# Performance work log

Measured on AMD Instinct MI355X. Metric: run time of the kernel, lower is better.

## Reference

```python
import jax, jax.numpy as jnp
import numpy as np

NDIR = 6      # build_tree.num_directions()
IDIM = 256
ODIM = 512
B, L, NCH = 8, 4096, 8192


def setup_inputs() -> dict:
    key = jax.random.key(0)
    ks = jax.random.split(key, 9)
    last = jax.random.normal(ks[0], (B, NCH, IDIM), dtype=jnp.float32)
    child_l = jax.random.randint(ks[1], (L,), 0, NCH, dtype=jnp.int32)
    child_r = jax.random.randint(ks[2], (L,), 0, NCH, dtype=jnp.int32)
    vec = jax.random.randint(ks[3], (B, L), 0, NCH, dtype=jnp.int32)
    drev = jax.random.randint(ks[4], (NCH,), 0, 2, dtype=jnp.int32)
    dmap = jax.random.randint(ks[5], (NCH,), 0, NDIR, dtype=jnp.int32)
    # merge FC params: ndir independent Linear(2*idim -> odim) + PReLU(init=relu_weight)
    scale = 1.0 / np.sqrt(2 * IDIM)
    W_merge = jax.random.uniform(ks[6], (NDIR, ODIM, 2 * IDIM), jnp.float32, -scale, scale)
    b_merge = jax.random.uniform(ks[7], (NDIR, ODIM), jnp.float32, -scale, scale)
    alpha_merge = jnp.full((NDIR,), 0.005, dtype=jnp.float32)  # PReLU weight (relu_weight)
    return {"last": last, "W_merge": W_merge, "b_merge": b_merge,
            "alpha_merge": alpha_merge, "child_l": child_l, "child_r": child_r,
            "vec": vec, "drev": drev, "dmap": dmap}


def reference(last, W_merge, b_merge, alpha_merge, child_l, child_r, vec, drev, dmap):
    # child gathers: [B, L, idim]
    lch = last[:, child_l]
    rch = last[:, child_r]
    # per-element direction-reverse blending
    d = drev[vec][:, :, None].astype(last.dtype)          # [B, L, 1]
    a = lch * (1.0 - d) + rch * d
    b = rch * (1.0 - d) + lch * d
    ans = jnp.concatenate([a, b], axis=-1)                # [B, L, 2*idim]
    # routed merge: compute all ndir linears, then select per element (ndir is small)
    y_all = jnp.einsum('bli,doi->bldo', ans, W_merge) + b_merge   # [B, L, ndir, odim]
    dir_idx = dmap[vec]                                   # [B, L] in [0, ndir)
    y = jnp.take_along_axis(y_all, dir_idx[:, :, None, None], axis=2)[:, :, 0]  # [B, L, odim]
    alpha = alpha_merge[dir_idx][:, :, None]              # per-element PReLU slope
    return jnp.where(y > 0, y, alpha * y)
```

## Files before the change

### kernel.cpp

```cpp
#include <hip/hip_runtime.h>
#include <hip/hip_bf16.h>

#define BB 8
#define LL 4096
#define NCH 8192
#define IDIM 256
#define KDIM 512
#define ODIM 512
#define NDIR 6
#define TOT (BB * LL)

#define CAP 8192
#define IDX_OFF 64
#define ROWS_OFF (64 + 8 * CAP)
#define WS_LAST_OFF (64 + 16 * CAP)
#define LAST_ELEMS (BB * NCH * IDIM)
#define W_ELEMS (NDIR * ODIM * KDIM)
#define N_LAST8 (LAST_ELEMS / 8)
#define N_W8 (W_ELEMS / 8)

#define GEMM_CHUNK 131

typedef short short8 __attribute__((ext_vector_type(8)));
typedef float floatx4 __attribute__((ext_vector_type(4)));

__device__ inline void async_copy16(const void* g, void* l) {
  __builtin_amdgcn_global_load_lds(
      (const __attribute__((address_space(1))) void*)g,
      (__attribute__((address_space(3))) void*)l, 16, 0, 0);
}

__device__ inline void cvt8(const float* __restrict__ src,
                            __hip_bfloat16* __restrict__ dst, int i) {
  const floatx4* s = (const floatx4*)src;
  floatx4 a = s[2 * i];
  floatx4 b = s[2 * i + 1];
  union { short8 v; __hip_bfloat16 h[8]; } u;
  u.h[0] = __float2bfloat16(a[0]); u.h[1] = __float2bfloat16(a[1]);
  u.h[2] = __float2bfloat16(a[2]); u.h[3] = __float2bfloat16(a[3]);
  u.h[4] = __float2bfloat16(b[0]); u.h[5] = __float2bfloat16(b[1]);
  u.h[6] = __float2bfloat16(b[2]); u.h[7] = __float2bfloat16(b[3]);
  ((short8*)dst)[i] = u.v;
}

__global__ __launch_bounds__(256) void prep_kernel(
    const float* __restrict__ last, const float* __restrict__ W,
    const int* __restrict__ vec, const int* __restrict__ child_l,
    const int* __restrict__ child_r, const int* __restrict__ drev,
    const int* __restrict__ dmap, int* __restrict__ ws) {
  __hip_bfloat16* last_bf = (__hip_bfloat16*)(ws + WS_LAST_OFF);
  __hip_bfloat16* W_bf = last_bf + LAST_ELEMS;
  int gid = blockIdx.x * 256 + threadIdx.x;
  if (gid < N_LAST8) {
    cvt8(last, last_bf, gid);
  } else if (gid < N_LAST8 + N_W8) {
    cvt8(W, W_bf, gid - N_LAST8);
  } else {
    __shared__ int lcnt[8];
    __shared__ int gbase[8];
    int tid = threadIdx.x;
    if (tid < 8) lcnt[tid] = 0;
    __syncthreads();
    int lin = gid - (N_LAST8 + N_W8);
    int l = lin & (LL - 1);
    int v = vec[lin];
    int dir = dmap[v] & 7;
    int sw = drev[v];
    int cl = child_l[l];
    int cr = child_r[l];
    int r0 = sw ? cr : cl;
    int r1 = sw ? cl : cr;
    int pos = atomicAdd(&lcnt[dir], 1);
    __syncthreads();
    if (tid < 8) gbase[tid] = lcnt[tid] ? atomicAdd(&ws[tid], lcnt[tid]) : 0;
    __syncthreads();
    int slot = dir * CAP + gbase[dir] + pos;
    ws[IDX_OFF + slot] = lin;
    ws[ROWS_OFF + slot] = r0 | (r1 << 16);
  }
}

__global__ __launch_bounds__(256, 4) void gemm_kernel(
    const float* __restrict__ bias, const float* __restrict__ alpha_m,
    const int* __restrict__ ws, float* __restrict__ out) {
  __shared__ __hip_bfloat16 Als[3][128 * 32];
  __shared__ __hip_bfloat16 Bls[2][128 * 32];

  int flat = blockIdx.y * 4 + blockIdx.x;
  int swz = (flat & 7) * GEMM_CHUNK + (flat >> 3);
  const int mt = swz >> 2;
  const int nt = swz & 3;

  int d = -1, count = 0, m_base = 0;
  {
    int tb = 0;
    for (int dd = 0; dd < 8; ++dd) {
      int c = ws[dd];
      int ntile = (c + 127) >> 7;
      if (mt < tb + ntile) { d = dd; count = c; m_base = (mt - tb) * 128; break; }
      tb += ntile;
    }
  }
  if (d < 0) return;

  const int* idxA = ws + IDX_OFF + d * CAP;
  const int* rowsA = ws + ROWS_OFF + d * CAP;
  const __hip_bfloat16* last_bf = (const __hip_bfloat16*)(ws + WS_LAST_OFF);
  const __hip_bfloat16* W_bf = last_bf + LAST_ELEMS;

  const int tid = threadIdx.x;
  const int wave = __builtin_amdgcn_readfirstlane(tid >> 6);
  const int lane = tid & 63;
  const int lane15 = lane & 15;
  const int quad = lane >> 4;
  const int wm = wave >> 1;
  const int wn = wave & 1;
  const int n_blk = nt * 128;

  const __hip_bfloat16* ap0[2];
  const __hip_bfloat16* ap1[2];
  const __hip_bfloat16* bp[2];
  int ldsoff[2];
  {
    const int lp = lane >> 3;
    const int up = (lane & 7) ^ lp;
    const int k16e = (up & 3) * 8;
#pragma unroll
    for (int i = 0; i < 2; ++i) {
      const int I = wave * 2 + i;
      ldsoff[i] = I * 512;
      int row_local = I * 16 + 2 * lp + (up >> 2);
      int gr = m_base + row_local;
      if (gr >= count) gr = count - 1;
      int lin = idxA[gr] & (TOT - 1);
      int rr = rowsA[gr];
      int b = lin >> 12;
      int r0 = rr & (NCH - 1);
      int r1 = (rr >> 16) & (NCH - 1);
      ap0[i] = last_bf + (long long)(b * NCH + r0) * IDIM + k16e;
      ap1[i] = last_bf + (long long)(b * NCH + r1) * IDIM + k16e;
      bp[i] = W_bf + (long long)(d * ODIM + n_blk + row_local) * KDIM + k16e;
    }
  }

#define STAGE_A(c, buf)                                               \
  {                                                                   \
    const int ko = ((c) & 7) * 32;                                    \
    _Pragma("unroll") for (int i = 0; i < 2; ++i)                     \
        async_copy16(((c) < 8 ? ap0[i] : ap1[i]) + ko,                \
                     &Als[(buf)][ldsoff[i]]);                         \
  }
#define STAGE_B(c, buf)                                               \
  {                                                                   \
    _Pragma("unroll") for (int i = 0; i < 2; ++i)                     \
        async_copy16(bp[i] + (c) * 32, &Bls[(buf)][ldsoff[i]]);       \
  }

  floatx4 acc[4][4] = {};
  const int t3 = lane15 >> 1;
  const int col8 = (((lane15 & 1) * 4 + quad) ^ t3) * 8;

  STAGE_B(0, 0);
  STAGE_A(0, 0);
  STAGE_A(1, 1);

#pragma unroll
  for (int c = 0; c < 16; ++c) {
    __builtin_amdgcn_s_barrier();
    if (c < 15) STAGE_B(c + 1, (c + 1) & 1);
    if (c < 14) STAGE_A(c + 2, (c + 2) % 3);
    if (c < 14) {
      asm volatile("s_waitcnt vmcnt(6)" ::: "memory");
    } else if (c == 14) {
      asm volatile("s_waitcnt vmcnt(4)" ::: "memory");
    } else {
      asm volatile("s_waitcnt vmcnt(0)" ::: "memory");
    }
    __builtin_amdgcn_sched_barrier(0);
    __builtin_amdgcn_s_barrier();

    const __hip_bfloat16* Ab = Als[c % 3];
    const __hip_bfloat16* Bb = Bls[c & 1];
    short8 a[4], b[4];
#pragma unroll
    for (int i = 0; i < 4; ++i)
      a[i] = *(const short8*)&Ab[(wm * 32 + i * 8 + t3) * 64 + col8];
#pragma unroll
    for (int j = 0; j < 4; ++j)
      b[j] = *(const short8*)&Bb[(wn * 32 + j * 8 + t3) * 64 + col8];
#pragma unroll
    for (int i = 0; i < 4; ++i)
#pragma unroll
      for (int j = 0; j < 4; ++j)
        acc[i][j] = __builtin_amdgcn_mfma_f32_16x16x32_bf16(a[i], b[j], acc[i][j], 0, 0, 0);
  }

  const float alpha = alpha_m[d];
  float bj[4];
#pragma unroll
  for (int j = 0; j < 4; ++j)
    bj[j] = bias[d * ODIM + n_blk + wn * 64 + j * 16 + lane15];

#pragma unroll
  for (int i = 0; i < 4; ++i) {
#pragma unroll
    for (int reg = 0; reg < 4; ++reg) {
      int row_id = m_base + wm * 64 + i * 16 + quad * 4 + reg;
      if (row_id >= count) continue;
      int lin = idxA[row_id] & (TOT - 1);
      float* orow = out + (long long)lin * ODIM + n_blk + wn * 64;
#pragma unroll
      for (int j = 0; j < 4; ++j) {
        float y = acc[i][j][reg] + bj[j];
        y = y > 0.f ? y : alpha * y;
        orow[j * 16 + lane15] = y;
      }
    }
  }
}

extern "C" void kernel_launch(void* const* d_in, const int* in_sizes, int n_in,
                              void* d_out, int out_size, void* d_ws, size_t ws_size,
                              hipStream_t stream) {
  const float* last = (const float*)d_in[0];
  const float* W = (const float*)d_in[1];
  const float* bias = (const float*)d_in[2];
  const float* alpha = (const float*)d_in[3];
  const int* child_l = (const int*)d_in[4];
  const int* child_r = (const int*)d_in[5];
  const int* vec = (const int*)d_in[6];
  const int* drev = (const int*)d_in[7];
  const int* dmap = (const int*)d_in[8];

  int* ws = (int*)d_ws;

  hipMemsetAsync(ws, 0, 64 * sizeof(int), stream);
  int prep_blocks = N_LAST8 / 256 + N_W8 / 256 + TOT / 256;
  prep_kernel<<<prep_blocks, 256, 0, stream>>>(last, W, vec, child_l, child_r,
                                               drev, dmap, ws);
  dim3 grid(ODIM / 128, TOT / 128 + NDIR, 1);
  gemm_kernel<<<grid, 256, 0, stream>>>(bias, alpha, ws, (float*)d_out);
}
```

Before: 163.3 us.

## Widen GEMM tile to 128x256 with XCD-aware 1D grid swizzle

Each gemm block now computes a 128x256 output tile instead of 128x128, so every gathered A row is loaded once per half of ODIM rather than once per quarter. Per-wave accumulators double to 4x8 MFMA tiles, B staging uses four async copies per thread into a larger LDS buffer, and the vmcnt waits are adjusted to match. The launch becomes a 1D grid of 524 blocks mapped to tiles so that neighbouring tiles land on the same XCD. Occupancy drops to 2 blocks per CU because of the higher register and LDS use, which risks poorer latency hiding.

```diff
diff --git a/kernel.cpp b/kernel.cpp
--- a/kernel.cpp
+++ b/kernel.cpp
@@ -19,7 +19,7 @@
 #define N_LAST8 (LAST_ELEMS / 8)
 #define N_W8 (W_ELEMS / 8)
 
-#define GEMM_CHUNK 131
+#define NWG 524
 
 typedef short short8 __attribute__((ext_vector_type(8)));
 typedef float floatx4 __attribute__((ext_vector_type(4)));
@@ -80,16 +80,17 @@
   }
 }
 
-__global__ __launch_bounds__(256, 4) void gemm_kernel(
+__global__ __launch_bounds__(256, 2) void gemm_kernel(
     const float* __restrict__ bias, const float* __restrict__ alpha_m,
     const int* __restrict__ ws, float* __restrict__ out) {
   __shared__ __hip_bfloat16 Als[3][128 * 32];
-  __shared__ __hip_bfloat16 Bls[2][128 * 32];
-
-  int flat = blockIdx.y * 4 + blockIdx.x;
-  int swz = (flat & 7) * GEMM_CHUNK + (flat >> 3);
-  const int mt = swz >> 2;
-  const int nt = swz & 3;
+  __shared__ __hip_bfloat16 Bls[2][256 * 32];
+
+  int flat = blockIdx.x;
+  int xcd = flat & 7;
+  int swz = (xcd < 4 ? xcd * 66 : 264 + (xcd - 4) * 65) + (flat >> 3);
+  const int mt = swz >> 1;
+  const int nt = swz & 1;
 
   int d = -1, count = 0, m_base = 0;
   {
@@ -115,12 +116,12 @@
   const int quad = lane >> 4;
   const int wm = wave >> 1;
   const int wn = wave & 1;
-  const int n_blk = nt * 128;
+  const int n_blk = nt * 256;
 
   const __hip_bfloat16* ap0[2];
   const __hip_bfloat16* ap1[2];
-  const __hip_bfloat16* bp[2];
-  int ldsoff[2];
+  const __hip_bfloat16* bp[4];
+  int ldsA[2], ldsB[4];
   {
     const int lp = lane >> 3;
     const int up = (lane & 7) ^ lp;
@@ -128,17 +129,21 @@
 #pragma unroll
     for (int i = 0; i < 2; ++i) {
       const int I = wave * 2 + i;
-      ldsoff[i] = I * 512;
+      ldsA[i] = I * 512;
       int row_local = I * 16 + 2 * lp + (up >> 2);
       int gr = m_base + row_local;
       if (gr >= count) gr = count - 1;
       int lin = idxA[gr] & (TOT - 1);
       int rr = rowsA[gr];
       int b = lin >> 12;
-      int r0 = rr & (NCH - 1);
-      int r1 = (rr >> 16) & (NCH - 1);
-      ap0[i] = last_bf + (long long)(b * NCH + r0) * IDIM + k16e;
-      ap1[i] = last_bf + (long long)(b * NCH + r1) * IDIM + k16e;
+      ap0[i] = last_bf + (long long)(b * NCH + (rr & (NCH - 1))) * IDIM + k16e;
+      ap1[i] = last_bf + (long long)(b * NCH + ((rr >> 16) & (NCH - 1))) * IDIM + k16e;
+    }
+#pragma unroll
+    for (int i = 0; i < 4; ++i) {
+      const int I = wave * 4 + i;
+      ldsB[i] = I * 512;
+      int row_local = I * 16 + 2 * lp + (up >> 2);
       bp[i] = W_bf + (long long)(d * ODIM + n_blk + row_local) * KDIM + k16e;
     }
   }
@@ -148,15 +153,15 @@
     const int ko = ((c) & 7) * 32;                                    \
     _Pragma("unroll") for (int i = 0; i < 2; ++i)                     \
         async_copy16(((c) < 8 ? ap0[i] : ap1[i]) + ko,                \
-                     &Als[(buf)][ldsoff[i]]);                         \
+                     &Als[(buf)][ldsA[i]]);                           \
   }
 #define STAGE_B(c, buf)                                               \
   {                                                                   \
-    _Pragma("unroll") for (int i = 0; i < 2; ++i)                     \
-        async_copy16(bp[i] + (c) * 32, &Bls[(buf)][ldsoff[i]]);       \
-  }
-
-  floatx4 acc[4][4] = {};
+    _Pragma("unroll") for (int i = 0; i < 4; ++i)                     \
+        async_copy16(bp[i] + (c) * 32, &Bls[(buf)][ldsB[i]]);         \
+  }
+
+  floatx4 acc[4][8] = {};
   const int t3 = lane15 >> 1;
   const int col8 = (((lane15 & 1) * 4 + quad) ^ t3) * 8;
 
@@ -170,9 +175,9 @@
     if (c < 15) STAGE_B(c + 1, (c + 1) & 1);
     if (c < 14) STAGE_A(c + 2, (c + 2) % 3);
     if (c < 14) {
+      asm volatile("s_waitcnt vmcnt(8)" ::: "memory");
+    } else if (c == 14) {
       asm volatile("s_waitcnt vmcnt(6)" ::: "memory");
-    } else if (c == 14) {
-      asm volatile("s_waitcnt vmcnt(4)" ::: "memory");
     } else {
       asm volatile("s_waitcnt vmcnt(0)" ::: "memory");
     }
@@ -181,25 +186,30 @@
 
     const __hip_bfloat16* Ab = Als[c % 3];
     const __hip_bfloat16* Bb = Bls[c & 1];
-    short8 a[4], b[4];
+    short8 a[4];
 #pragma unroll
     for (int i = 0; i < 4; ++i)
       a[i] = *(const short8*)&Ab[(wm * 32 + i * 8 + t3) * 64 + col8];
 #pragma unroll
-    for (int j = 0; j < 4; ++j)
-      b[j] = *(const short8*)&Bb[(wn * 32 + j * 8 + t3) * 64 + col8];
-#pragma unroll
-    for (int i = 0; i < 4; ++i)
+    for (int jg = 0; jg < 2; ++jg) {
+      short8 b[4];
 #pragma unroll
       for (int j = 0; j < 4; ++j)
-        acc[i][j] = __builtin_amdgcn_mfma_f32_16x16x32_bf16(a[i], b[j], acc[i][j], 0, 0, 0);
+        b[j] = *(const short8*)&Bb[(wn * 64 + (jg * 4 + j) * 8 + t3) * 64 + col8];
+#pragma unroll
+      for (int i = 0; i < 4; ++i)
+#pragma unroll
+        for (int j = 0; j < 4; ++j)
+          acc[i][jg * 4 + j] =
+              __builtin_amdgcn_mfma_f32_16x16x32_bf16(a[i], b[j], acc[i][jg * 4 + j], 0, 0, 0);
+    }
   }
 
   const float alpha = alpha_m[d];
-  float bj[4];
-#pragma unroll
-  for (int j = 0; j < 4; ++j)
-    bj[j] = bias[d * ODIM + n_blk + wn * 64 + j * 16 + lane15];
+  float bj[8];
+#pragma unroll
+  for (int j = 0; j < 8; ++j)
+    bj[j] = bias[d * ODIM + n_blk + wn * 128 + j * 16 + lane15];
 
 #pragma unroll
   for (int i = 0; i < 4; ++i) {
@@ -208,9 +218,9 @@
       int row_id = m_base + wm * 64 + i * 16 + quad * 4 + reg;
       if (row_id >= count) continue;
       int lin = idxA[row_id] & (TOT - 1);
-      float* orow = out + (long long)lin * ODIM + n_blk + wn * 64;
-#pragma unroll
-      for (int j = 0; j < 4; ++j) {
+      float* orow = out + (long long)lin * ODIM + n_blk + wn * 128;
+#pragma unroll
+      for (int j = 0; j < 8; ++j) {
         float y = acc[i][j][reg] + bj[j];
         y = y > 0.f ? y : alpha * y;
         orow[j * 16 + lane15] = y;
@@ -238,6 +248,5 @@
   int prep_blocks = N_LAST8 / 256 + N_W8 / 256 + TOT / 256;
   prep_kernel<<<prep_blocks, 256, 0, stream>>>(last, W, vec, child_l, child_r,
                                                drev, dmap, ws);
-  dim3 grid(ODIM / 128, TOT / 128 + NDIR, 1);
-  gemm_kernel<<<grid, 256, 0, stream>>>(bias, alpha, ws, (float*)d_out);
-}
+  gemm_kernel<<<NWG, 256, 0, stream>>>(bias, alpha, ws, (float*)d_out);
+}
```

After: 167.4 us. 1.03x slower.
